# Optimization experiments

Hardware: AMD Instinct MI355X
Metric: run time of the kernel (lower is better)

Reference implementation:

```python
import jax, jax.numpy as jnp
import numpy as np
from jax import lax

MODEL_DIM = 384
KERNEL = 15
PAD = (KERNEL - 1) // 2
BATCH = 4096


def fake_quant(x, bits):
    """Per-tensor symmetric fake quantization with straight-through estimator.
    scale = max|x| / qmax, q = clip(round(x/scale), qmin, qmax), dq = q*scale.
    """
    qmax = float(2 ** (bits - 1) - 1)
    qmin = -float(2 ** (bits - 1))
    scale = jnp.maximum(jnp.max(jnp.abs(x)) / qmax, jnp.asarray(1e-8, x.dtype))
    dq = jnp.clip(jnp.round(x / scale), qmin, qmax) * scale
    return x + lax.stop_gradient(dq - x)  # STE: identity gradient


def setup_inputs() -> dict:
    key = jax.random.key(0)
    k = jax.random.split(key, 7)
    image = jax.random.normal(k[0], (BATCH, 28, 28), dtype=jnp.float32)
    # LinearQuant(28 -> model_dim)
    W1 = jax.random.normal(k[1], (MODEL_DIM, 28), dtype=jnp.float32) * (1.0 / np.sqrt(28))
    b1 = jax.random.normal(k[2], (MODEL_DIM,), dtype=jnp.float32) * 0.01
    # depthwise Conv1DQuant(model_dim, model_dim, K, groups=model_dim): weight [C_out, 1, K]
    Wc = jax.random.normal(k[3], (MODEL_DIM, 1, KERNEL), dtype=jnp.float32) * (1.0 / np.sqrt(KERNEL))
    bc = jax.random.normal(k[4], (MODEL_DIM,), dtype=jnp.float32) * 0.01
    # LinearQuant(28*model_dim -> 10)
    Wf = jax.random.normal(k[5], (10, 28 * MODEL_DIM), dtype=jnp.float32) * (1.0 / np.sqrt(28 * MODEL_DIM))
    bf = jax.random.normal(k[6], (10,), dtype=jnp.float32) * 0.01
    return {"image": image, "W1": W1, "b1": b1, "Wc": Wc, "bc": bc, "Wf": Wf, "bf": bf}


def reference(image, W1, b1, Wc, bc, Wf, bf):
    inp = image.reshape(-1, 28, 28)
    # linear_1 with 8-bit activation fake-quant in and 3-bit weight fake-quant
    x = fake_quant(inp, 8)
    lin = jnp.einsum('blf,of->blo', x, fake_quant(W1, 3)) + b1  # [B,28,model_dim]
    out1 = jnp.tanh(fake_quant(lin, 8))
    # depthwise conv1d over length 28, channels model_dim
    xc = jnp.transpose(fake_quant(out1, 8), (0, 2, 1))  # [B,C,L]
    conv = lax.conv_general_dilated(
        xc, fake_quant(Wc, 3), window_strides=(1,), padding=[(PAD, PAD)],
        dimension_numbers=('NCH', 'OIH', 'NCH'), feature_group_count=MODEL_DIM)
    conv = conv + bc[None, :, None]                      # [B,C,L]
    conv = jnp.transpose(conv, (0, 2, 1))                # [B,L,C]
    out2 = jnp.tanh(fake_quant(conv, 8)).reshape(-1, MODEL_DIM * 28)
    # final linear
    logits = fake_quant(out2, 8) @ fake_quant(Wf, 3).T + bf  # [B,10]
    return fake_quant(logits, 8)
```

## Files before the change

### kernel.cpp

```cpp
#include <hip/hip_runtime.h>

#define BATCH 4096
#define MD 384
#define KW 15
#define PADW 7
#define LSEQ 28
#define FIN 28

#define NX (BATCH*LSEQ*FIN)


#define B_SCF  0
#define B_LUT1 256
#define B_LUT2 512
#define B_PT0  4096
#define B_PT1  36864
#define B_PT2  45056
#define B_PTL  94208
#define B_W1B  95232
#define B_WCQ  119808
#define B_WFB  125952
#define B_LGI  298240
#define B_LG   1346816
#define B_XQB  1510656
#define B_BX   8850688

typedef __bf16 bf16x8 __attribute__((ext_vector_type(8)));
typedef float f32x4 __attribute__((ext_vector_type(4)));
typedef int i32x4 __attribute__((ext_vector_type(4)));

#if __has_builtin(__builtin_amdgcn_sdot4)
#define SDOT4(a,b,c) __builtin_amdgcn_sdot4((a),(b),(c),false)
#else
__device__ __forceinline__ int SDOT4(int a,int b,int c){
  c += ((a<<24)>>24)*((b<<24)>>24);
  c += ((a<<16)>>24)*((b<<16)>>24);
  c += ((a<<8)>>24)*((b<<8)>>24);
  c += (a>>24)*(b>>24);
  return c;
}
#endif

#if __has_builtin(__builtin_amdgcn_alignbyte)
#define ALIGNB(hi,lo,s) __builtin_amdgcn_alignbyte((hi),(lo),(s))
#else
#define ALIGNB(hi,lo,s) ((int)(((unsigned)(lo)>>(8*(s)))|((unsigned)(hi)<<(32-8*(s)))))
#endif

__device__ __forceinline__ unsigned short f2bf(float f){
  return (unsigned short)(__float_as_uint(f)>>16);
}

__device__ __forceinline__ void blkStore4(float m0,float m1,float m2,float m3,float4* dst){
  #pragma unroll
  for(int off=32;off;off>>=1){
    m0=fmaxf(m0,__shfl_xor(m0,off,64));
    m1=fmaxf(m1,__shfl_xor(m1,off,64));
    m2=fmaxf(m2,__shfl_xor(m2,off,64));
    m3=fmaxf(m3,__shfl_xor(m3,off,64));
  }
  __shared__ float sm[4][4];
  int wid=threadIdx.x>>6;
  if((threadIdx.x&63)==0){sm[wid][0]=m0;sm[wid][1]=m1;sm[wid][2]=m2;sm[wid][3]=m3;}
  __syncthreads();
  if(threadIdx.x==0){
    for(int i=1;i<4;i++){
      m0=fmaxf(m0,sm[i][0]);m1=fmaxf(m1,sm[i][1]);
      m2=fmaxf(m2,sm[i][2]);m3=fmaxf(m3,sm[i][3]);
    }
    *dst=make_float4(m0,m1,m2,m3);
  }
}

__device__ __forceinline__ void blkStoreMM(float mn,float mx,float2* dst){
  #pragma unroll
  for(int off=32;off;off>>=1){
    mn=fminf(mn,__shfl_xor(mn,off,64));
    mx=fmaxf(mx,__shfl_xor(mx,off,64));
  }
  __shared__ float smn[8],smx[8];
  int wid=threadIdx.x>>6, nw=blockDim.x>>6;
  if((threadIdx.x&63)==0){smn[wid]=mn;smx[wid]=mx;}
  __syncthreads();
  if(threadIdx.x==0){
    for(int i=1;i<nw;i++){mn=fminf(mn,smn[i]);mx=fmaxf(mx,smx[i]);}
    *dst=make_float2(mn,mx);
  }
}

__global__ __launch_bounds__(256)
void k_maxabs_in(const float* __restrict__ img,const float* __restrict__ W1,
                 const float* __restrict__ Wc,const float* __restrict__ Wf,
                 float4* __restrict__ pt0){
  float m0=0.f,m1=0.f,m2=0.f,m3=0.f;
  const int N4=NX/4;
  const int NW1=MD*FIN, NWC=MD*KW, NWF=10*MD*LSEQ;
  const int total=N4+NW1+NWC+NWF;
  const float4* img4=(const float4*)img;
  for(int i=blockIdx.x*blockDim.x+threadIdx.x;i<total;i+=gridDim.x*blockDim.x){
    if(i<N4){
      float4 v=img4[i];
      m0=fmaxf(m0,fmaxf(fmaxf(fabsf(v.x),fabsf(v.y)),fmaxf(fabsf(v.z),fabsf(v.w))));
    }
    else if(i<N4+NW1) m1=fmaxf(m1,fabsf(W1[i-N4]));
    else if(i<N4+NW1+NWC) m2=fmaxf(m2,fabsf(Wc[i-N4-NW1]));
    else m3=fmaxf(m3,fabsf(Wf[i-N4-NW1-NWC]));
  }
  blkStore4(m0,m1,m2,m3,&pt0[blockIdx.x]);
}

__global__ __launch_bounds__(256)
void k_red0(const float4* __restrict__ pt,float* __restrict__ scf){
  int t=threadIdx.x;
  float m0=0.f,m1=0.f,m2=0.f,m3=0.f;
  for(int i=t;i<2048;i+=256){
    float4 v=pt[i];
    m0=fmaxf(m0,v.x);m1=fmaxf(m1,v.y);m2=fmaxf(m2,v.z);m3=fmaxf(m3,v.w);
  }
  #pragma unroll
  for(int off=32;off;off>>=1){
    m0=fmaxf(m0,__shfl_xor(m0,off,64));
    m1=fmaxf(m1,__shfl_xor(m1,off,64));
    m2=fmaxf(m2,__shfl_xor(m2,off,64));
    m3=fmaxf(m3,__shfl_xor(m3,off,64));
  }
  __shared__ float sm[4][4];
  int wid=t>>6;
  if((t&63)==0){sm[wid][0]=m0;sm[wid][1]=m1;sm[wid][2]=m2;sm[wid][3]=m3;}
  __syncthreads();
  if(t==0){
    for(int i=1;i<4;i++){
      m0=fmaxf(m0,sm[i][0]);m1=fmaxf(m1,sm[i][1]);
      m2=fmaxf(m2,sm[i][2]);m3=fmaxf(m3,sm[i][3]);
    }
    scf[0]=fmaxf(m0/127.f,1e-8f);
    scf[1]=fmaxf(m1/3.f,1e-8f);
    scf[2]=fmaxf(m2/3.f,1e-8f);
    scf[3]=fmaxf(m3/3.f,1e-8f);
  }
}

__global__ __launch_bounds__(256)
void k_redmm(const float2* __restrict__ pt,int n,float* __restrict__ scf,
             int preIdx,int outIdx,char* __restrict__ lutg){
  int t=threadIdx.x;
  float mn=1e30f,mx=-1e30f;
  for(int i=t;i<n;i+=256){
    float2 v=pt[i];
    mn=fminf(mn,v.x); mx=fmaxf(mx,v.y);
  }
  #pragma unroll
  for(int off=32;off;off>>=1){
    mn=fminf(mn,__shfl_xor(mn,off,64));
    mx=fmaxf(mx,__shfl_xor(mx,off,64));
  }
  __shared__ float smn[4],smx[4];
  __shared__ float bs,bso;
  int wid=t>>6;
  if((t&63)==0){smn[wid]=mn;smx[wid]=mx;}
  __syncthreads();
  if(t==0){
    for(int i=1;i<4;i++){mn=fminf(mn,smn[i]);mx=fmaxf(mx,smx[i]);}
    float ma=fmaxf(fabsf(mn),fabsf(mx));
    float s=fmaxf(ma/127.f,1e-8f);
    float a1=fabsf(fminf(fmaxf(rintf(mn/s),-128.f),127.f)*s);
    float a2=fabsf(fminf(fmaxf(rintf(mx/s),-128.f),127.f)*s);
    float so=fmaxf(tanhf(fmaxf(a1,a2))/127.f,1e-8f);
    scf[preIdx]=s; scf[outIdx]=so;
    bs=s; bso=so;
  }
  __syncthreads();
  float d=(float)(t-128)*bs;
  lutg[t]=(char)(int)fminf(fmaxf(rintf(tanhf(d)/bso),-128.f),127.f);
}

__global__ __launch_bounds__(256)
void k_prep(const float* __restrict__ img,const float* __restrict__ W1,
            const float* __restrict__ Wc,const float* __restrict__ Wf,
            const float* __restrict__ scf,char* __restrict__ wsb){
  float s_img=scf[0], s_w1=scf[1], s_wc=scf[2], s_wf=scf[3];
  float inv_img=1.f/s_img;
  unsigned short* xqb=(unsigned short*)(wsb+B_XQB);
  unsigned short* w1b=(unsigned short*)(wsb+B_W1B);
  char* wcpk=wsb+B_WCQ;
  char* wfb=wsb+B_WFB;
  const int T0=BATCH*LSEQ*32;
  const int T1=T0+MD*32;
  const int T2=T1+MD*16;
  const int T3=T2+168*1024;
  for(int i=blockIdx.x*blockDim.x+threadIdx.x;i<T3;i+=gridDim.x*blockDim.x){
    if(i<T0){
      int row=i>>5, cc=i&31;
      float q = cc<FIN ? fminf(fmaxf(rintf(img[row*FIN+cc]*inv_img),-128.f),127.f) : 0.f;
      xqb[i]=f2bf(q);
    } else if(i<T1){
      int j=i-T0; int o=j>>5, cc=j&31;
      float q = cc<FIN ? fminf(fmaxf(rintf(W1[o*FIN+cc]/s_w1),-4.f),3.f) : 0.f;
      w1b[j]=f2bf(q);
    } else if(i<T2){
      int j=i-T1; int c=j>>4, k=j&15;
      char q=0;
      if(k<KW) q=(char)(int)fminf(fmaxf(rintf(Wc[c*KW+k]/s_wc),-4.f),3.f);
      wcpk[j]=q;
    } else {
      int j=i-T2;
      int s=j>>10, l=(j>>4)&63, jj=j&15;
      int n=l&15, k=s*64+((l>>4)<<4)+jj;
      char q=0;
      if(n<10){
        int c=k/28, ls=k-c*28;
        q=(char)(int)fminf(fmaxf(rintf(Wf[n*10752+ls*MD+c]/s_wf),-4.f),3.f);
      }
      wfb[j]=q;
    }
  }
}

template<bool WRITE>
__global__ __launch_bounds__(512)
void k_g1(const unsigned short* __restrict__ xqb,const unsigned short* __restrict__ w1b,
          const float* __restrict__ b1,const float* __restrict__ scf,
          const char* __restrict__ lutg,float2* __restrict__ pt1,
          int* __restrict__ bxi){
  __shared__ char ldsraw[43456];
  __shared__ char lut1[256];
  unsigned short* Wlds=(unsigned short*)ldsraw;
  int t=threadIdx.x, wid=t>>6, lane=t&63, l4=lane>>4, l15=lane&15;
  {
    const int* src=(const int*)w1b; int* dst=(int*)ldsraw;
    for(int i=t;i<6144;i+=512) dst[i]=src[i];
  }
  __syncthreads();
  bf16x8 bfr[3]; float b1v[3];
  #pragma unroll
  for(int ni=0;ni<3;ni++){
    int o=(wid*3+ni)*16+l15;
    bfr[ni]=*(const bf16x8*)&Wlds[o*32+l4*8];
    b1v[ni]=b1[o];
  }
  bf16x8 af[7];
  int r0=blockIdx.x*112;
  #pragma unroll
  for(int mt=0;mt<7;mt++)
    af[mt]=*(const bf16x8*)&xqb[(size_t)(r0+mt*16+l15)*32+l4*8];
  float sg=scf[0]*scf[1];
  float inv_lin=1.f;
  if constexpr(WRITE){
    inv_lin=1.f/scf[4];
    if(t<64) ((int*)lut1)[t]=((const int*)lutg)[t];
    __syncthreads();
  }
  char* Xt=ldsraw;
  float mn=1e30f,mx=-1e30f;
  f32x4 zero={0.f,0.f,0.f,0.f};
  #pragma unroll
  for(int ni=0;ni<3;ni++){
    #pragma unroll
    for(int mt=0;mt<7;mt++){
      f32x4 acc=__builtin_amdgcn_mfma_f32_16x16x32_bf16(af[mt],bfr[ni],zero,0,0,0);
      #pragma unroll
      for(int r=0;r<4;r++){
        float v=sg*acc[r]+b1v[ni];
        if constexpr(WRITE){
          int ql=(int)fminf(fmaxf(rintf(v*inv_lin),-128.f),127.f);
          int q=(int)lut1[ql+128];
          int row=mt*16+l4*4+r;
          int o=(wid*3+ni)*16+l15;
          Xt[row*388+o]=(char)q;
        } else {
          mn=fminf(mn,v); mx=fmaxf(mx,v);
        }
      }
    }
  }
  if constexpr(WRITE){
    __syncthreads();
    int b0=blockIdx.x*4;
    for(int i=t;i<10752;i+=512){
      int bl=i/2688, rem=i-bl*2688;
      int o=rem/7, g=rem-o*7;
      int base=(bl*28+g*4)*388+o;
      unsigned w=(unsigned)(unsigned char)Xt[base]
               |((unsigned)(unsigned char)Xt[base+388])<<8
               |((unsigned)(unsigned char)Xt[base+776])<<16
               |((unsigned)(unsigned char)Xt[base+1164])<<24;
      bxi[(size_t)(b0+bl)*2688+o*7+g]=(int)w;
    }
  } else {
    blkStoreMM(mn,mx,&pt1[blockIdx.x]);
  }
}

template<bool WRITE>
__global__ __launch_bounds__(256)
void k_conv(int* __restrict__ bxi,const char* __restrict__ wcpk,
            const float* __restrict__ bc,const float* __restrict__ scf,
            const char* __restrict__ lutg,float2* __restrict__ pt2){
  __shared__ int rows[1792];
  __shared__ char lut[256];
  int t=threadIdx.x;
  int tid0=blockIdx.x*256;
  int base=tid0*7;
  #pragma unroll
  for(int i=0;i<7;i++) rows[i*256+t]=bxi[base+i*256+t];

  float sfac=scf[5]*scf[2];
  float inv_cv=1.f;
  if constexpr(WRITE){
    inv_cv=1.f/scf[6];
    if(t<64) ((int*)lut)[t]=((const int*)lutg)[t];
  }
  __syncthreads();

  int c=(tid0+t)%MD;
  i32x4 wq=*(const i32x4*)(wcpk+(size_t)c*16);
  float bias=bc[c];
  int ext[11];
  ext[0]=0; ext[1]=0; ext[9]=0; ext[10]=0;
  #pragma unroll
  for(int j=0;j<7;j++) ext[2+j]=rows[t*7+j];

  float mn=1e30f,mx=-1e30f;
  unsigned ow[7];
  #pragma unroll
  for(int l=0;l<LSEQ;l++){
    const int eb=l+1, bi=eb>>2, s=eb&3;
    int A0,A1,A2,A3;
    if(s==0){A0=ext[bi];A1=ext[bi+1];A2=ext[bi+2];A3=ext[bi+3];}
    else{
      A0=ALIGNB(ext[bi+1],ext[bi],s);
      A1=ALIGNB(ext[bi+2],ext[bi+1],s);
      A2=ALIGNB(ext[bi+3],ext[bi+2],s);
      A3=ALIGNB(ext[bi+4],ext[bi+3],s);
    }
    int idot=SDOT4(A0,wq[0],SDOT4(A1,wq[1],SDOT4(A2,wq[2],SDOT4(A3,wq[3],0))));
    float v=fmaf((float)idot,sfac,bias);
    if constexpr(WRITE){
      int qc=(int)fminf(fmaxf(rintf(v*inv_cv),-128.f),127.f);
      unsigned q2=(unsigned)(unsigned char)lut[qc+128];
      if((l&3)==0) ow[l>>2]=q2;
      else ow[l>>2]|=q2<<(8*(l&3));
    } else {
      mn=fminf(mn,v); mx=fmaxf(mx,v);
    }
  }
  if constexpr(WRITE){
    #pragma unroll
    for(int j=0;j<7;j++) rows[t*7+j]=(int)ow[j];
    __syncthreads();
    #pragma unroll
    for(int i=0;i<7;i++) bxi[base+i*256+t]=rows[i*256+t];
  } else {
    blkStoreMM(mn,mx,&pt2[blockIdx.x]);
  }
}

__global__ __launch_bounds__(64)
void k_gemm2(const char* __restrict__ bxb,const char* __restrict__ wfb,
             int* __restrict__ lgint){
  int mt=blockIdx.x>>2, kp=blockIdx.x&3;
  int lane=threadIdx.x, l4=lane>>4, l15=lane&15;
  const char* ap=bxb+(size_t)(mt*16+l15)*10752+l4*16;
  const char* bp=wfb+lane*16;
  i32x4 acc={0,0,0,0};
  int s0=kp*42;
  #pragma unroll 6
  for(int s=s0;s<s0+42;++s){
    i32x4 a=*(const i32x4*)(ap+(size_t)s*64);
    i32x4 b=*(const i32x4*)(bp+(size_t)s*1024);
    acc=__builtin_amdgcn_mfma_i32_16x16x64_i8(a,b,acc,0,0,0);
  }
  int* dst=lgint+kp*65536;
  int rbase=mt*16+l4*4;
  #pragma unroll
  for(int r=0;r<4;r++) dst[(rbase+r)*16+l15]=acc[r];
}

__global__ __launch_bounds__(256)
void k_logmax(const int* __restrict__ lgint,const float* __restrict__ bfv,
              const float* __restrict__ scf,float* __restrict__ lg,
              float* __restrict__ ptl){
  int i=blockIdx.x*256+threadIdx.x;
  float s=scf[3]*scf[7];
  int b=i/10, o=i-b*10;
  int sum=lgint[b*16+o]+lgint[65536+b*16+o]+lgint[131072+b*16+o]+lgint[196608+b*16+o];
  float v=s*(float)sum+bfv[o];
  lg[i]=v;
  float m=fabsf(v);
  #pragma unroll
  for(int off=32;off;off>>=1) m=fmaxf(m,__shfl_xor(m,off,64));
  __shared__ float sm[4];
  int wid=threadIdx.x>>6;
  if((threadIdx.x&63)==0) sm[wid]=m;
  __syncthreads();
  if(threadIdx.x==0){
    for(int k=1;k<4;k++) m=fmaxf(m,sm[k]);
    ptl[blockIdx.x]=m;
  }
}

__global__ __launch_bounds__(256)
void k_final(const float* __restrict__ lg,const float* __restrict__ ptl,
             float* __restrict__ out){
  int t=threadIdx.x;
  float m=(t<160)?ptl[t]:0.f;
  #pragma unroll
  for(int off=32;off;off>>=1) m=fmaxf(m,__shfl_xor(m,off,64));
  __shared__ float sm[4];
  __shared__ float sv;
  int wid=t>>6;
  if((t&63)==0) sm[wid]=m;
  __syncthreads();
  if(t==0){
    for(int k=1;k<4;k++) m=fmaxf(m,sm[k]);
    sv=fmaxf(m/127.f,1e-8f);
  }
  __syncthreads();
  float s=sv;
  int i=blockIdx.x*256+t;
  out[i]=fminf(fmaxf(rintf(lg[i]/s),-128.f),127.f)*s;
}

extern "C" void kernel_launch(void* const* d_in, const int* in_sizes, int n_in,
                              void* d_out, int out_size, void* d_ws, size_t ws_size,
                              hipStream_t stream){
  const float* img=(const float*)d_in[0];
  const float* W1 =(const float*)d_in[1];
  const float* b1 =(const float*)d_in[2];
  const float* Wc =(const float*)d_in[3];
  const float* bc =(const float*)d_in[4];
  const float* Wf =(const float*)d_in[5];
  const float* bf =(const float*)d_in[6];
  float* out=(float*)d_out;
  char* wsb=(char*)d_ws;
  float* scf=(float*)(wsb+B_SCF);
  float4* pt0=(float4*)(wsb+B_PT0);
  float2* pt1=(float2*)(wsb+B_PT1);
  float2* pt2=(float2*)(wsb+B_PT2);
  float* ptl=(float*)(wsb+B_PTL);
  int* lgint=(int*)(wsb+B_LGI);
  float* lg=(float*)(wsb+B_LG);
  int* bxi=(int*)(wsb+B_BX);

  k_maxabs_in<<<2048,256,0,stream>>>(img,W1,Wc,Wf,pt0);
  k_red0<<<1,256,0,stream>>>(pt0,scf);
  k_prep<<<4096,256,0,stream>>>(img,W1,Wc,Wf,scf,wsb);
  k_g1<false><<<1024,512,0,stream>>>((const unsigned short*)(wsb+B_XQB),
                                     (const unsigned short*)(wsb+B_W1B),b1,scf,
                                     nullptr,pt1,nullptr);
  k_redmm<<<1,256,0,stream>>>(pt1,1024,scf,4,5,wsb+B_LUT1);
  k_g1<true ><<<1024,512,0,stream>>>((const unsigned short*)(wsb+B_XQB),
                                     (const unsigned short*)(wsb+B_W1B),b1,scf,
                                     wsb+B_LUT1,nullptr,bxi);
  k_conv<false><<<6144,256,0,stream>>>(bxi,wsb+B_WCQ,bc,scf,nullptr,pt2);
  k_redmm<<<1,256,0,stream>>>(pt2,6144,scf,6,7,wsb+B_LUT2);
  k_conv<true ><<<6144,256,0,stream>>>(bxi,wsb+B_WCQ,bc,scf,wsb+B_LUT2,nullptr);
  k_gemm2<<<1024,64,0,stream>>>((const char*)bxi,wsb+B_WFB,lgint);
  k_logmax<<<160,256,0,stream>>>(lgint,bf,scf,lg,ptl);
  k_final<<<160,256,0,stream>>>(lg,ptl,out);
}
```

Before: 118.3 us.

## Fuse GEMM1, depthwise conv and final GEMM into one recomputing kernel

Replaces the separate GEMM1-write, conv min/max, conv-write, int8 GEMM2 and logit reduction kernels with a single templated kernel run in three modes. Each mode recomputes GEMM1 from the quantized inputs and keeps per-block activations in LDS, so the 44 MB intermediate buffer no longer makes global round trips. The final linear layer becomes an SDOT4 reduction with wave shuffles instead of MFMA. In exchange it repeats GEMM1 and the conv across passes, uses about 43 KB of LDS per block (which may lower occupancy), and does GEMM2 on the scalar dot path.

```diff
diff --git a/kernel.cpp b/kernel.cpp
--- a/kernel.cpp
+++ b/kernel.cpp
@@ -13,17 +13,15 @@
 #define B_SCF  0
 #define B_LUT1 256
 #define B_LUT2 512
-#define B_PT0  4096
-#define B_PT1  36864
-#define B_PT2  45056
-#define B_PTL  94208
-#define B_W1B  95232
-#define B_WCQ  119808
-#define B_WFB  125952
-#define B_LGI  298240
-#define B_LG   1346816
-#define B_XQB  1510656
-#define B_BX   8850688
+#define B_PT0  1024
+#define B_PT1  33792
+#define B_PT2  41984
+#define B_PTL  50176
+#define B_W1B  54272
+#define B_WCQ  78848
+#define B_WFB  84992
+#define B_LG   192512
+#define B_XQB  356352
 
 typedef __bf16 bf16x8 __attribute__((ext_vector_type(8)));
 typedef float f32x4 __attribute__((ext_vector_type(4)));
@@ -187,7 +185,7 @@
   const int T0=BATCH*LSEQ*32;
   const int T1=T0+MD*32;
   const int T2=T1+MD*16;
-  const int T3=T2+168*1024;
+  const int T3=T2+10*10752;
   for(int i=blockIdx.x*blockDim.x+threadIdx.x;i<T3;i+=gridDim.x*blockDim.x){
     if(i<T0){
       int row=i>>5, cc=i&31;
@@ -204,33 +202,33 @@
       wcpk[j]=q;
     } else {
       int j=i-T2;
-      int s=j>>10, l=(j>>4)&63, jj=j&15;
-      int n=l&15, k=s*64+((l>>4)<<4)+jj;
-      char q=0;
-      if(n<10){
-        int c=k/28, ls=k-c*28;
-        q=(char)(int)fminf(fmaxf(rintf(Wf[n*10752+ls*MD+c]/s_wf),-4.f),3.f);
-      }
-      wfb[j]=q;
-    }
-  }
-}
-
-template<bool WRITE>
+      int n=j/10752, r=j-n*10752;
+      int c=r/28, l=r-c*28;
+      wfb[j]=(char)(int)fminf(fmaxf(rintf(Wf[n*10752+l*MD+c]/s_wf),-4.f),3.f);
+    }
+  }
+}
+
+template<int MODE>
 __global__ __launch_bounds__(512)
-void k_g1(const unsigned short* __restrict__ xqb,const unsigned short* __restrict__ w1b,
-          const float* __restrict__ b1,const float* __restrict__ scf,
-          const char* __restrict__ lutg,float2* __restrict__ pt1,
-          int* __restrict__ bxi){
-  __shared__ char ldsraw[43456];
-  __shared__ char lut1[256];
-  unsigned short* Wlds=(unsigned short*)ldsraw;
+void k_fused(const unsigned short* __restrict__ xqb,const unsigned short* __restrict__ w1b,
+             const float* __restrict__ b1,const float* __restrict__ scf,
+             const char* __restrict__ lut1g,const char* __restrict__ lut2g,
+             const char* __restrict__ wcpk,const float* __restrict__ bc,
+             const int* __restrict__ wfw,const float* __restrict__ bfv,
+             float2* __restrict__ ptmm,float* __restrict__ lg,
+             float* __restrict__ ptl){
+  __shared__ int ldsI[10752];
+  __shared__ int psum[10][4][7];
+  __shared__ char lutA[256];
+  __shared__ char lutB[256];
   int t=threadIdx.x, wid=t>>6, lane=t&63, l4=lane>>4, l15=lane&15;
   {
-    const int* src=(const int*)w1b; int* dst=(int*)ldsraw;
-    for(int i=t;i<6144;i+=512) dst[i]=src[i];
-  }
-  __syncthreads();
+    const int* src=(const int*)w1b;
+    for(int i=t;i<6144;i+=512) ldsI[i]=src[i];
+  }
+  __syncthreads();
+  unsigned short* Wlds=(unsigned short*)ldsI;
   bf16x8 bfr[3]; float b1v[3];
   #pragma unroll
   for(int ni=0;ni<3;ni++){
@@ -244,158 +242,147 @@
   for(int mt=0;mt<7;mt++)
     af[mt]=*(const bf16x8*)&xqb[(size_t)(r0+mt*16+l15)*32+l4*8];
   float sg=scf[0]*scf[1];
-  float inv_lin=1.f;
-  if constexpr(WRITE){
+  float inv_lin=1.f, inv_cv=1.f, sfac=1.f, gsc=1.f;
+  if constexpr(MODE>=1){
     inv_lin=1.f/scf[4];
-    if(t<64) ((int*)lut1)[t]=((const int*)lutg)[t];
-    __syncthreads();
-  }
-  char* Xt=ldsraw;
+    sfac=scf[5]*scf[2];
+    if(t<64) ((int*)lutA)[t]=((const int*)lut1g)[t];
+  }
+  if constexpr(MODE==2){
+    inv_cv=1.f/scf[6];
+    gsc=scf[3]*scf[7];
+    if(t>=64&&t<128) ((int*)lutB)[t-64]=((const int*)lut2g)[t-64];
+  }
+  if constexpr(MODE>=1) __syncthreads();
+
   float mn=1e30f,mx=-1e30f;
   f32x4 zero={0.f,0.f,0.f,0.f};
   #pragma unroll
   for(int ni=0;ni<3;ni++){
+    int o=(wid*3+ni)*16+l15;
     #pragma unroll
     for(int mt=0;mt<7;mt++){
       f32x4 acc=__builtin_amdgcn_mfma_f32_16x16x32_bf16(af[mt],bfr[ni],zero,0,0,0);
-      #pragma unroll
-      for(int r=0;r<4;r++){
-        float v=sg*acc[r]+b1v[ni];
-        if constexpr(WRITE){
-          int ql=(int)fminf(fmaxf(rintf(v*inv_lin),-128.f),127.f);
-          int q=(int)lut1[ql+128];
-          int row=mt*16+l4*4+r;
-          int o=(wid*3+ni)*16+l15;
-          Xt[row*388+o]=(char)q;
-        } else {
+      if constexpr(MODE==0){
+        #pragma unroll
+        for(int r=0;r<4;r++){
+          float v=sg*acc[r]+b1v[ni];
           mn=fminf(mn,v); mx=fmaxf(mx,v);
         }
-      }
-    }
-  }
-  if constexpr(WRITE){
-    __syncthreads();
-    int b0=blockIdx.x*4;
-    for(int i=t;i<10752;i+=512){
-      int bl=i/2688, rem=i-bl*2688;
-      int o=rem/7, g=rem-o*7;
-      int base=(bl*28+g*4)*388+o;
-      unsigned w=(unsigned)(unsigned char)Xt[base]
-               |((unsigned)(unsigned char)Xt[base+388])<<8
-               |((unsigned)(unsigned char)Xt[base+776])<<16
-               |((unsigned)(unsigned char)Xt[base+1164])<<24;
-      bxi[(size_t)(b0+bl)*2688+o*7+g]=(int)w;
-    }
-  } else {
-    blkStoreMM(mn,mx,&pt1[blockIdx.x]);
-  }
-}
-
-template<bool WRITE>
-__global__ __launch_bounds__(256)
-void k_conv(int* __restrict__ bxi,const char* __restrict__ wcpk,
-            const float* __restrict__ bc,const float* __restrict__ scf,
-            const char* __restrict__ lutg,float2* __restrict__ pt2){
-  __shared__ int rows[1792];
-  __shared__ char lut[256];
-  int t=threadIdx.x;
-  int tid0=blockIdx.x*256;
-  int base=tid0*7;
-  #pragma unroll
-  for(int i=0;i<7;i++) rows[i*256+t]=bxi[base+i*256+t];
-
-  float sfac=scf[5]*scf[2];
-  float inv_cv=1.f;
-  if constexpr(WRITE){
-    inv_cv=1.f/scf[6];
-    if(t<64) ((int*)lut)[t]=((const int*)lutg)[t];
-  }
-  __syncthreads();
-
-  int c=(tid0+t)%MD;
-  i32x4 wq=*(const i32x4*)(wcpk+(size_t)c*16);
-  float bias=bc[c];
-  int ext[11];
-  ext[0]=0; ext[1]=0; ext[9]=0; ext[10]=0;
-  #pragma unroll
-  for(int j=0;j<7;j++) ext[2+j]=rows[t*7+j];
-
-  float mn=1e30f,mx=-1e30f;
-  unsigned ow[7];
-  #pragma unroll
-  for(int l=0;l<LSEQ;l++){
-    const int eb=l+1, bi=eb>>2, s=eb&3;
-    int A0,A1,A2,A3;
-    if(s==0){A0=ext[bi];A1=ext[bi+1];A2=ext[bi+2];A3=ext[bi+3];}
-    else{
-      A0=ALIGNB(ext[bi+1],ext[bi],s);
-      A1=ALIGNB(ext[bi+2],ext[bi+1],s);
-      A2=ALIGNB(ext[bi+3],ext[bi+2],s);
-      A3=ALIGNB(ext[bi+4],ext[bi+3],s);
-    }
-    int idot=SDOT4(A0,wq[0],SDOT4(A1,wq[1],SDOT4(A2,wq[2],SDOT4(A3,wq[3],0))));
-    float v=fmaf((float)idot,sfac,bias);
-    if constexpr(WRITE){
-      int qc=(int)fminf(fmaxf(rintf(v*inv_cv),-128.f),127.f);
-      unsigned q2=(unsigned)(unsigned char)lut[qc+128];
-      if((l&3)==0) ow[l>>2]=q2;
-      else ow[l>>2]|=q2<<(8*(l&3));
-    } else {
-      mn=fminf(mn,v); mx=fmaxf(mx,v);
-    }
-  }
-  if constexpr(WRITE){
-    #pragma unroll
-    for(int j=0;j<7;j++) rows[t*7+j]=(int)ow[j];
-    __syncthreads();
-    #pragma unroll
-    for(int i=0;i<7;i++) bxi[base+i*256+t]=rows[i*256+t];
-  } else {
-    blkStoreMM(mn,mx,&pt2[blockIdx.x]);
-  }
-}
-
-__global__ __launch_bounds__(64)
-void k_gemm2(const char* __restrict__ bxb,const char* __restrict__ wfb,
-             int* __restrict__ lgint){
-  int mt=blockIdx.x>>2, kp=blockIdx.x&3;
-  int lane=threadIdx.x, l4=lane>>4, l15=lane&15;
-  const char* ap=bxb+(size_t)(mt*16+l15)*10752+l4*16;
-  const char* bp=wfb+lane*16;
-  i32x4 acc={0,0,0,0};
-  int s0=kp*42;
-  #pragma unroll 6
-  for(int s=s0;s<s0+42;++s){
-    i32x4 a=*(const i32x4*)(ap+(size_t)s*64);
-    i32x4 b=*(const i32x4*)(bp+(size_t)s*1024);
-    acc=__builtin_amdgcn_mfma_i32_16x16x64_i8(a,b,acc,0,0,0);
-  }
-  int* dst=lgint+kp*65536;
-  int rbase=mt*16+l4*4;
-  #pragma unroll
-  for(int r=0;r<4;r++) dst[(rbase+r)*16+l15]=acc[r];
-}
-
-__global__ __launch_bounds__(256)
-void k_logmax(const int* __restrict__ lgint,const float* __restrict__ bfv,
-              const float* __restrict__ scf,float* __restrict__ lg,
-              float* __restrict__ ptl){
-  int i=blockIdx.x*256+threadIdx.x;
-  float s=scf[3]*scf[7];
-  int b=i/10, o=i-b*10;
-  int sum=lgint[b*16+o]+lgint[65536+b*16+o]+lgint[131072+b*16+o]+lgint[196608+b*16+o];
-  float v=s*(float)sum+bfv[o];
-  lg[i]=v;
-  float m=fabsf(v);
-  #pragma unroll
-  for(int off=32;off;off>>=1) m=fmaxf(m,__shfl_xor(m,off,64));
-  __shared__ float sm[4];
-  int wid=threadIdx.x>>6;
-  if((threadIdx.x&63)==0) sm[wid]=m;
-  __syncthreads();
-  if(threadIdx.x==0){
-    for(int k=1;k<4;k++) m=fmaxf(m,sm[k]);
-    ptl[blockIdx.x]=m;
+      } else {
+        unsigned w=0;
+        #pragma unroll
+        for(int r=0;r<4;r++){
+          float v=sg*acc[r]+b1v[ni];
+          int ql=(int)fminf(fmaxf(rintf(v*inv_lin),-128.f),127.f);
+          unsigned q=(unsigned)(unsigned char)lutA[ql+128];
+          w|=q<<(8*r);
+        }
+        ldsI[o*28+mt*4+l4]=(int)w;
+      }
+    }
+  }
+  if constexpr(MODE==0){
+    blkStoreMM(mn,mx,&ptmm[blockIdx.x]);
+    return;
+  }
+  __syncthreads();
+
+  int oww[3][7];
+  float mnc=1e30f,mxc=-1e30f;
+  #pragma unroll
+  for(int rr=0;rr<3;rr++){
+    int j=t+rr*512;
+    int s=j/384, c=j-s*384;
+    i32x4 wq=*(const i32x4*)(wcpk+(size_t)c*16);
+    float bias=bc[c];
+    int ext[11];
+    ext[0]=0; ext[1]=0; ext[9]=0; ext[10]=0;
+    #pragma unroll
+    for(int i=0;i<7;i++) ext[2+i]=ldsI[c*28+s*7+i];
+    #pragma unroll
+    for(int l=0;l<LSEQ;l++){
+      const int eb=l+1, bi=eb>>2, sh=eb&3;
+      int A0,A1,A2,A3;
+      if(sh==0){A0=ext[bi];A1=ext[bi+1];A2=ext[bi+2];A3=ext[bi+3];}
+      else{
+        A0=ALIGNB(ext[bi+1],ext[bi],sh);
+        A1=ALIGNB(ext[bi+2],ext[bi+1],sh);
+        A2=ALIGNB(ext[bi+3],ext[bi+2],sh);
+        A3=ALIGNB(ext[bi+4],ext[bi+3],sh);
+      }
+      int idot=SDOT4(A0,wq[0],SDOT4(A1,wq[1],SDOT4(A2,wq[2],SDOT4(A3,wq[3],0))));
+      float v=fmaf((float)idot,sfac,bias);
+      if constexpr(MODE==1){
+        mnc=fminf(mnc,v); mxc=fmaxf(mxc,v);
+      } else {
+        int qc=(int)fminf(fmaxf(rintf(v*inv_cv),-128.f),127.f);
+        unsigned q2=(unsigned)(unsigned char)lutB[qc+128];
+        if((l&3)==0) oww[rr][l>>2]=(int)q2;
+        else oww[rr][l>>2]|=(int)(q2<<(8*(l&3)));
+      }
+    }
+  }
+  if constexpr(MODE==1){
+    blkStoreMM(mnc,mxc,&ptmm[blockIdx.x]);
+    return;
+  }
+
+  __syncthreads();
+  #pragma unroll
+  for(int rr=0;rr<3;rr++){
+    int j=t+rr*512;
+    int s=j/384, c=j-s*384;
+    #pragma unroll
+    for(int i=0;i<7;i++) ldsI[s*2688+c*7+i]=oww[rr][i];
+  }
+  __syncthreads();
+
+  if(t<448){
+    int cwv[24];
+    #pragma unroll
+    for(int s=0;s<4;s++)
+      #pragma unroll
+      for(int j6=0;j6<6;j6++) cwv[s*6+j6]=ldsI[s*2688+j6*448+t];
+    #pragma unroll
+    for(int o=0;o<10;o++){
+      int a0=0,a1=0,a2=0,a3=0;
+      #pragma unroll
+      for(int j6=0;j6<6;j6++){
+        int wfv=wfw[o*2688+j6*448+t];
+        a0=SDOT4(cwv[0*6+j6],wfv,a0);
+        a1=SDOT4(cwv[1*6+j6],wfv,a1);
+        a2=SDOT4(cwv[2*6+j6],wfv,a2);
+        a3=SDOT4(cwv[3*6+j6],wfv,a3);
+      }
+      #pragma unroll
+      for(int off=32;off;off>>=1){
+        a0+=__shfl_xor(a0,off,64);
+        a1+=__shfl_xor(a1,off,64);
+        a2+=__shfl_xor(a2,off,64);
+        a3+=__shfl_xor(a3,off,64);
+      }
+      if(lane==0){
+        psum[o][0][wid]=a0; psum[o][1][wid]=a1;
+        psum[o][2][wid]=a2; psum[o][3][wid]=a3;
+      }
+    }
+  }
+  __syncthreads();
+  float m=0.f;
+  if(t<40){
+    int s=t/10, o=t-s*10;
+    int sum=0;
+    #pragma unroll
+    for(int i=0;i<7;i++) sum+=psum[o][s][i];
+    float v=fmaf((float)sum,gsc,bfv[o]);
+    lg[(blockIdx.x*4+s)*10+o]=v;
+    m=fabsf(v);
+  }
+  if(t<64){
+    #pragma unroll
+    for(int off=32;off;off>>=1) m=fmaxf(m,__shfl_xor(m,off,64));
+    if(t==0) ptl[blockIdx.x]=m;
   }
 }
 
@@ -403,7 +390,8 @@
 void k_final(const float* __restrict__ lg,const float* __restrict__ ptl,
              float* __restrict__ out){
   int t=threadIdx.x;
-  float m=(t<160)?ptl[t]:0.f;
+  float m=0.f;
+  for(int i=t;i<1024;i+=256) m=fmaxf(m,ptl[i]);
   #pragma unroll
   for(int off=32;off;off>>=1) m=fmaxf(m,__shfl_xor(m,off,64));
   __shared__ float sm[4];
@@ -438,24 +426,19 @@
   float2* pt1=(float2*)(wsb+B_PT1);
   float2* pt2=(float2*)(wsb+B_PT2);
   float* ptl=(float*)(wsb+B_PTL);
-  int* lgint=(int*)(wsb+B_LGI);
   float* lg=(float*)(wsb+B_LG);
-  int* bxi=(int*)(wsb+B_BX);
+  const unsigned short* xqb=(const unsigned short*)(wsb+B_XQB);
+  const unsigned short* w1b=(const unsigned short*)(wsb+B_W1B);
+  const char* wcpk=wsb+B_WCQ;
+  const int* wfw=(const int*)(wsb+B_WFB);
 
   k_maxabs_in<<<2048,256,0,stream>>>(img,W1,Wc,Wf,pt0);
   k_red0<<<1,256,0,stream>>>(pt0,scf);
   k_prep<<<4096,256,0,stream>>>(img,W1,Wc,Wf,scf,wsb);
-  k_g1<false><<<1024,512,0,stream>>>((const unsigned short*)(wsb+B_XQB),
-                                     (const unsigned short*)(wsb+B_W1B),b1,scf,
-                                     nullptr,pt1,nullptr);
+  k_fused<0><<<1024,512,0,stream>>>(xqb,w1b,b1,scf,nullptr,nullptr,wcpk,bc,wfw,bf,pt1,nullptr,nullptr);
   k_redmm<<<1,256,0,stream>>>(pt1,1024,scf,4,5,wsb+B_LUT1);
-  k_g1<true ><<<1024,512,0,stream>>>((const unsigned short*)(wsb+B_XQB),
-                                     (const unsigned short*)(wsb+B_W1B),b1,scf,
-                                     wsb+B_LUT1,nullptr,bxi);
-  k_conv<false><<<6144,256,0,stream>>>(bxi,wsb+B_WCQ,bc,scf,nullptr,pt2);
-  k_redmm<<<1,256,0,stream>>>(pt2,6144,scf,6,7,wsb+B_LUT2);
-  k_conv<true ><<<6144,256,0,stream>>>(bxi,wsb+B_WCQ,bc,scf,wsb+B_LUT2,nullptr);
-  k_gemm2<<<1024,64,0,stream>>>((const char*)bxi,wsb+B_WFB,lgint);
-  k_logmax<<<160,256,0,stream>>>(lgint,bf,scf,lg,ptl);
+  k_fused<1><<<1024,512,0,stream>>>(xqb,w1b,b1,scf,wsb+B_LUT1,nullptr,wcpk,bc,wfw,bf,pt2,nullptr,nullptr);
+  k_redmm<<<1,256,0,stream>>>(pt2,1024,scf,6,7,wsb+B_LUT2);
+  k_fused<2><<<1024,512,0,stream>>>(xqb,w1b,b1,scf,wsb+B_LUT1,wsb+B_LUT2,wcpk,bc,wfw,bf,nullptr,lg,ptl);
   k_final<<<160,256,0,stream>>>(lg,ptl,out);
 }
```

After: 107.7 us. 8.9% less time.
